# Kernel tuning notes

Measured on AMD Instinct MI355X. Metric: run time of the kernel, lower is better.

Reference implementation:

```python
import jax, jax.numpy as jnp
import numpy as np

HIDDEN = 3072
NUM_HEADS = 24
HEAD_DIM = HIDDEN // NUM_HEADS  # 128
MLP_HIDDEN = 4 * HIDDEN         # 12288
SEQ = 2048


def setup_inputs() -> dict:
    key = jax.random.key(0)
    ks = jax.random.split(key, 12)
    s = 0.02
    return {
        "x": jax.random.normal(ks[0], (1, SEQ, HIDDEN), jnp.float32),
        "vec": jax.random.normal(ks[1], (1, HIDDEN), jnp.float32),
        "pe": jax.random.normal(ks[2], (1, 1, SEQ, HEAD_DIM // 2, 2, 2), jnp.float32),
        "mod_w": jax.random.normal(ks[3], (HIDDEN, 3 * HIDDEN), jnp.float32) * s,
        "mod_b": jnp.zeros((3 * HIDDEN,), jnp.float32),
        "lin1_w": jax.random.normal(ks[4], (HIDDEN, 3 * HIDDEN + MLP_HIDDEN), jnp.float32) * s,
        "lin1_b": jnp.zeros((3 * HIDDEN + MLP_HIDDEN,), jnp.float32),
        "lin2_w": jax.random.normal(ks[5], (HIDDEN + MLP_HIDDEN, HIDDEN), jnp.float32) * s,
        "lin2_b": jnp.zeros((HIDDEN,), jnp.float32),
        "q_scale": jnp.ones((HEAD_DIM,), jnp.float32),
        "k_scale": jnp.ones((HEAD_DIM,), jnp.float32),
    }


def _forward(x, vec, pe, mod_w, mod_b, lin1_w, lin1_b, lin2_w, lin2_b, q_scale, k_scale):
    B, L, H = x.shape
    NH, HD = NUM_HEADS, HEAD_DIM

    # Modulation: lin(silu(vec)) -> shift, scale, gate  (flux Modulation, double=False)
    mod = jnp.dot(jax.nn.silu(vec), mod_w) + mod_b          # (B, 3H)
    shift, scale, gate = jnp.split(mod, 3, axis=-1)
    shift, scale, gate = shift[:, None, :], scale[:, None, :], gate[:, None, :]

    # LayerNorm (no affine, eps=1e-6) + scale/shift modulation
    mu = jnp.mean(x, axis=-1, keepdims=True)
    var = jnp.mean((x - mu) ** 2, axis=-1, keepdims=True)
    xn = (x - mu) * jax.lax.rsqrt(var + 1e-6)
    x_mod = (1.0 + scale) * xn + shift

    # Fused QKV + MLP projection
    h = jnp.dot(x_mod, lin1_w) + lin1_b                     # (B, L, 3H + MLP)
    qkv, mlp = h[..., : 3 * H], h[..., 3 * H :]
    qkv = qkv.reshape(B, L, 3, NH, HD).transpose(2, 0, 3, 1, 4)  # (3, B, NH, L, HD)
    q, k, v = qkv[0], qkv[1], qkv[2]

    # QKNorm: RMSNorm over head_dim with learned scale (eps=1e-6)
    def rms(t, s):
        return t * jax.lax.rsqrt(jnp.mean(t * t, axis=-1, keepdims=True) + 1e-6) * s

    q = rms(q, q_scale)
    k = rms(k, k_scale)

    # Rotary embedding: pe is (B, 1, L, HD/2, 2, 2) of rotation matrix rows
    def rope(t):
        tr = t.reshape(B, NH, L, HD // 2, 1, 2)
        out = pe[..., 0] * tr[..., 0] + pe[..., 1] * tr[..., 1]  # (B, NH, L, HD/2, 2)
        return out.reshape(B, NH, L, HD)

    q, k = rope(q), rope(k)

    # Scaled dot-product attention (default 1/sqrt(HD) scale)
    scores = jnp.einsum("bhqd,bhkd->bhqk", q, k) / jnp.sqrt(jnp.float32(HD))
    attn = jnp.einsum("bhqk,bhkd->bhqd", jax.nn.softmax(scores, axis=-1), v)
    attn = attn.transpose(0, 2, 1, 3).reshape(B, L, H)

    # GELU(tanh) MLP branch, concat, output projection, gated residual
    mlp_act = jax.nn.gelu(mlp, approximate=True)
    out = jnp.dot(jnp.concatenate([attn, mlp_act], axis=-1), lin2_w) + lin2_b
    return x + gate * out


def reference(x, vec, pe, mod_w, mod_b, lin1_w, lin1_b, lin2_w, lin2_b, q_scale, k_scale):
    return _forward(x, vec, pe, mod_w, mod_b, lin1_w, lin1_b, lin2_w, lin2_b, q_scale, k_scale)
```

## Files before the change

kernel.cpp:

```cpp
#include <hip/hip_runtime.h>
#include <hip/hip_bf16.h>
#include <stdint.h>

#define SEQ   2048
#define HID   3072
#define NHEADS 24
#define HDIM  128
#define MLPD  12288
#define NCOL1 21504
#define NCOL2 15360
#define MOD3  9216
#define QKVW  9216
#define KSPLIT 8

typedef __attribute__((ext_vector_type(4))) float f32x4;
typedef __attribute__((ext_vector_type(8))) short bf16x8;
typedef __attribute__((ext_vector_type(4))) unsigned short u16x4;
typedef __attribute__((ext_vector_type(2))) unsigned short u16x2;

__device__ __forceinline__ unsigned short f2bf(float f){
  unsigned u = __float_as_uint(f);
  u = (u + 0x7fffu + ((u >> 16) & 1u)) >> 16;
  return (unsigned short)u;
}
__device__ __forceinline__ float bf2f(unsigned short u){
  return __uint_as_float(((unsigned)u) << 16);
}

__device__ __forceinline__ void gload_lds16(const void* g, void* l){
  __builtin_amdgcn_global_load_lds(
      (const __attribute__((address_space(1))) unsigned int*)g,
      (__attribute__((address_space(3))) unsigned int*)l, 16, 0, 0);
}

__device__ __forceinline__ float gelu_tanh(float x){
  float u = 0.7978845608028654f * (x + 0.044715f * x * x * x);
  float t = 1.f - 2.f / (__expf(2.f * u) + 1.f);
  return 0.5f * x * (1.f + t);
}

__global__ void silu_kernel(const float* __restrict__ vec, float* __restrict__ sv){
  int i = blockIdx.x * 256 + threadIdx.x;
  if (i < HID){ float v = vec[i]; sv[i] = v / (1.f + __expf(-v)); }
}

__global__ void mod_gemv(const float* __restrict__ sv, const float* __restrict__ W,
                         const float* __restrict__ b, float* __restrict__ mod){
  int n  = blockIdx.x * 32 + (threadIdx.x & 31);
  int ks = threadIdx.x >> 5;
  float acc = 0.f;
  int k0 = ks * 384;
  #pragma unroll 4
  for (int k = k0; k < k0 + 384; ++k)
    acc += sv[k] * W[(size_t)k * MOD3 + n];
  __shared__ float red[8][32];
  red[ks][threadIdx.x & 31] = acc;
  __syncthreads();
  if (ks == 0){
    float a = 0.f;
    #pragma unroll
    for (int i = 0; i < 8; ++i) a += red[i][threadIdx.x & 31];
    mod[n] = a + b[n];
  }
}

__global__ __launch_bounds__(256)
void ln_mod_kernel(const float* __restrict__ x, const float* __restrict__ mod,
                   unsigned short* __restrict__ xmod){
  int l = blockIdx.x, t = threadIdx.x;
  const float* row = x + (size_t)l * HID;
  f32x4 v[3];
  float s = 0.f, s2 = 0.f;
  #pragma unroll
  for (int i = 0; i < 3; ++i){
    v[i] = *(const f32x4*)(row + (t + i * 256) * 4);
    #pragma unroll
    for (int j = 0; j < 4; ++j){ s += v[i][j]; s2 += v[i][j] * v[i][j]; }
  }
  #pragma unroll
  for (int m = 1; m < 64; m <<= 1){ s += __shfl_xor(s, m, 64); s2 += __shfl_xor(s2, m, 64); }
  __shared__ float red[8];
  int wv = t >> 6, ln = t & 63;
  if (ln == 0){ red[wv] = s; red[4 + wv] = s2; }
  __syncthreads();
  s  = red[0] + red[1] + red[2] + red[3];
  s2 = red[4] + red[5] + red[6] + red[7];
  float mu  = s * (1.f / HID);
  float var = s2 * (1.f / HID) - mu * mu;
  float rs  = rsqrtf(var + 1e-6f);
  #pragma unroll
  for (int i = 0; i < 3; ++i){
    int c = (t + i * 256) * 4;
    f32x4 sh = *(const f32x4*)(mod + c);
    f32x4 sc = *(const f32x4*)(mod + HID + c);
    u16x4 o;
    #pragma unroll
    for (int j = 0; j < 4; ++j){
      float xn = (v[i][j] - mu) * rs;
      o[j] = f2bf((1.f + sc[j]) * xn + sh[j]);
    }
    *(u16x4*)(xmod + (size_t)l * HID + c) = o;
  }
}

__global__ __launch_bounds__(256)
void transpose_f2b(const float* __restrict__ in, unsigned short* __restrict__ out,
                   int R, int C){
  __shared__ float tile[64][65];
  int rt = blockIdx.y * 64, ct = blockIdx.x * 64;
  int t = threadIdx.x;
  int r0 = t >> 4, c0 = (t & 15) * 4;
  #pragma unroll
  for (int ph = 0; ph < 4; ++ph){
    int r = r0 + ph * 16;
    f32x4 v = *(const f32x4*)(in + (size_t)(rt + r) * C + ct + c0);
    tile[r][c0 + 0] = v[0]; tile[r][c0 + 1] = v[1];
    tile[r][c0 + 2] = v[2]; tile[r][c0 + 3] = v[3];
  }
  __syncthreads();
  #pragma unroll
  for (int ph = 0; ph < 4; ++ph){
    int r = r0 + ph * 16;
    u16x4 o;
    #pragma unroll
    for (int i = 0; i < 4; ++i) o[i] = f2bf(tile[c0 + i][r]);
    *(u16x4*)(out + (size_t)(ct + r) * R + rt + c0) = o;
  }
}

__global__ __launch_bounds__(256)
void transpose_b2b_head(const unsigned short* __restrict__ in,
                        unsigned short* __restrict__ out, int R, int C){
  __shared__ unsigned short tile[64][68];
  int h = blockIdx.z;
  const unsigned short* inh = in + (size_t)h * R * C;
  unsigned short* outh = out + (size_t)h * R * C;
  int rt = blockIdx.y * 64, ct = blockIdx.x * 64;
  int t = threadIdx.x;
  int r0 = t >> 4, c0 = (t & 15) * 4;
  #pragma unroll
  for (int ph = 0; ph < 4; ++ph){
    int r = r0 + ph * 16;
    u16x4 v = *(const u16x4*)(inh + (size_t)(rt + r) * C + ct + c0);
    tile[r][c0 + 0] = v[0]; tile[r][c0 + 1] = v[1];
    tile[r][c0 + 2] = v[2]; tile[r][c0 + 3] = v[3];
  }
  __syncthreads();
  #pragma unroll
  for (int ph = 0; ph < 4; ++ph){
    int r = r0 + ph * 16;
    u16x4 o;
    #pragma unroll
    for (int i = 0; i < 4; ++i) o[i] = tile[c0 + i][r];
    *(u16x4*)(outh + (size_t)(ct + r) * R + rt + c0) = o;
  }
}

__global__ void qkv_prep(const unsigned short* __restrict__ hq, const float* __restrict__ pe,
                         const float* __restrict__ qscale, const float* __restrict__ kscale,
                         unsigned short* __restrict__ qb, unsigned short* __restrict__ kb,
                         unsigned short* __restrict__ vb){
  int l = blockIdx.x, hh = blockIdx.y, lane = threadIdx.x;
  const unsigned short* row = hq + (size_t)l * QKVW;
  int d = lane * 2;
  u16x2 qv = *(const u16x2*)(row + hh * HDIM + d);
  u16x2 kv = *(const u16x2*)(row + HID + hh * HDIM + d);
  u16x2 vv = *(const u16x2*)(row + 2 * HID + hh * HDIM + d);
  float qx = bf2f(qv[0]), qy = bf2f(qv[1]);
  float kx = bf2f(kv[0]), ky = bf2f(kv[1]);
  float sq = qx * qx + qy * qy;
  float sk = kx * kx + ky * ky;
  #pragma unroll
  for (int m = 1; m < 64; m <<= 1){ sq += __shfl_xor(sq, m, 64); sk += __shfl_xor(sk, m, 64); }
  float rq = rsqrtf(sq * (1.f / HDIM) + 1e-6f);
  float rk = rsqrtf(sk * (1.f / HDIM) + 1e-6f);
  float2 qs2 = *(const float2*)(qscale + d);
  float2 ks2 = *(const float2*)(kscale + d);
  float q0 = qx * rq * qs2.x, q1 = qy * rq * qs2.y;
  float k0 = kx * rk * ks2.x, k1 = ky * rk * ks2.y;
  f32x4 p4 = *(const f32x4*)(pe + (size_t)l * 256 + lane * 4);
  const float sscl = 0.08838834764831845f;
  float qo0 = (p4[0] * q0 + p4[1] * q1) * sscl;
  float qo1 = (p4[2] * q0 + p4[3] * q1) * sscl;
  float ko0 =  p4[0] * k0 + p4[1] * k1;
  float ko1 =  p4[2] * k0 + p4[3] * k1;
  size_t base = ((size_t)hh * SEQ + l) * HDIM + d;
  u16x2 o;
  o[0] = f2bf(qo0); o[1] = f2bf(qo1); *(u16x2*)(qb + base) = o;
  o[0] = f2bf(ko0); o[1] = f2bf(ko1); *(u16x2*)(kb + base) = o;
  o[0] = vv[0];     o[1] = vv[1];     *(u16x2*)(vb + base) = o;
}

template<int EPI>
__global__ __launch_bounds__(512)
void gemm256(const unsigned short* __restrict__ A, const unsigned short* __restrict__ BT,
             const float* __restrict__ bias, unsigned short* __restrict__ out0,
             unsigned short* __restrict__ out1,
             int M, int N, int ldA, int ldB, int kchunk){
  __shared__ unsigned short Ls[65536];
  int nxy = gridDim.x * gridDim.y;
  int nwg = nxy * gridDim.z;
  int fid = (blockIdx.z * gridDim.y + blockIdx.y) * gridDim.x + blockIdx.x;
  int nid = (fid & 7) * (nwg >> 3) + (fid >> 3);
  int ksz = nid / nxy, rem = nid % nxy;
  int bm  = rem % gridDim.y, bn = rem / gridDim.y;
  int k0 = ksz * kchunk;
  int nk = kchunk >> 6;
  int tid = threadIdx.x, wave = tid >> 6, lane = tid & 63, lg = lane >> 4, lr = lane & 15;
  int wr = wave >> 2, wc = wave & 3;

  int G0 = tid, G1 = tid + 512;
  int r0 = G0 >> 2, r1 = G1 >> 2;
  int c0 = ((G0 & 3) ^ ((r0 >> 1) & 3)) * 8;
  int c1 = ((G1 & 3) ^ ((r1 >> 1) & 3)) * 8;
  const unsigned short* A0 = A  + (size_t)(bm * 256 + r0) * ldA + k0 + c0;
  const unsigned short* A1 = A  + (size_t)(bm * 256 + r1) * ldA + k0 + c1;
  const unsigned short* B0 = BT + (size_t)(bn * 256 + r0) * ldB + k0 + c0;
  const unsigned short* B1 = BT + (size_t)(bn * 256 + r1) * ldB + k0 + c1;
  unsigned short* LA = Ls;
  unsigned short* LB = Ls + 32768;
  int d0 = (wave * 64) * 8, d1 = (512 + wave * 64) * 8;

  auto stageA = [&](int t, int kh){
    unsigned short* h = LA + (((t & 1) * 2 + kh) << 13);
    int kc = t * 64 + kh * 32;
    gload_lds16(A0 + kc, h + d0);
    gload_lds16(A1 + kc, h + d1);
  };
  auto stageB = [&](int t, int kh){
    unsigned short* h = LB + (((t & 1) * 2 + kh) << 13);
    int kc = t * 64 + kh * 32;
    gload_lds16(B0 + kc, h + d0);
    gload_lds16(B1 + kc, h + d1);
  };

  int offA[8], offB[4];
  #pragma unroll
  for (int m = 0; m < 8; ++m){
    int row = wr * 128 + m * 16 + lr;
    offA[m] = row * 32 + ((lg ^ ((row >> 1) & 3)) * 8);
  }
  #pragma unroll
  for (int n = 0; n < 4; ++n){
    int row = wc * 64 + n * 16 + lr;
    offB[n] = row * 32 + ((lg ^ ((row >> 1) & 3)) * 8);
  }

  const f32x4 fz = 0.0f;
  f32x4 acc[8][4];
  #pragma unroll
  for (int i = 0; i < 8; ++i)
    #pragma unroll
    for (int j = 0; j < 4; ++j) acc[i][j] = fz;

  stageA(0, 0); stageB(0, 0); stageA(0, 1); stageB(0, 1); stageA(1, 0); stageB(1, 0);
  asm volatile("s_waitcnt vmcnt(8)" ::: "memory");
  __builtin_amdgcn_s_barrier();
  __builtin_amdgcn_sched_barrier(0);

  for (int t = 0; t < nk; ++t){
    const unsigned short* Ah = LA + (((t & 1) * 2) << 13);
    const unsigned short* Bh = LB + (((t & 1) * 2) << 13);
    bf16x8 a_[4], b_[4];
    if (t + 1 < nk) stageA(t + 1, 1);
    #pragma unroll
    for (int m = 0; m < 4; ++m) a_[m] = *(const bf16x8*)&Ah[offA[m]];
    #pragma unroll
    for (int n = 0; n < 4; ++n) b_[n] = *(const bf16x8*)&Bh[offB[n]];
    __builtin_amdgcn_sched_barrier(0);
    __builtin_amdgcn_s_barrier();
    asm volatile("s_waitcnt lgkmcnt(0)" ::: "memory");
    __builtin_amdgcn_sched_barrier(0);
    __builtin_amdgcn_s_setprio(1);
    #pragma unroll
    for (int m = 0; m < 4; ++m)
      #pragma unroll
      for (int n = 0; n < 4; ++n)
        acc[m][n] = __builtin_amdgcn_mfma_f32_16x16x32_bf16(a_[m], b_[n], acc[m][n], 0, 0, 0);
    __builtin_amdgcn_s_setprio(0);
    __builtin_amdgcn_sched_barrier(0);
    __builtin_amdgcn_s_barrier();
    if (t + 1 < nk) stageB(t + 1, 1);
    #pragma unroll
    for (int m = 0; m < 4; ++m) a_[m] = *(const bf16x8*)&Ah[offA[m + 4]];
    __builtin_amdgcn_sched_barrier(0);
    if (t == nk - 1) asm volatile("s_waitcnt vmcnt(0)" ::: "memory");
    else             asm volatile("s_waitcnt vmcnt(8)" ::: "memory");
    __builtin_amdgcn_s_barrier();
    asm volatile("s_waitcnt lgkmcnt(0)" ::: "memory");
    __builtin_amdgcn_sched_barrier(0);
    __builtin_amdgcn_s_setprio(1);
    #pragma unroll
    for (int m = 0; m < 4; ++m)
      #pragma unroll
      for (int n = 0; n < 4; ++n)
        acc[m + 4][n] = __builtin_amdgcn_mfma_f32_16x16x32_bf16(a_[m], b_[n], acc[m + 4][n], 0, 0, 0);
    __builtin_amdgcn_s_setprio(0);
    __builtin_amdgcn_sched_barrier(0);
    __builtin_amdgcn_s_barrier();
    if (t + 2 < nk) stageA(t + 2, 0);
    #pragma unroll
    for (int m = 0; m < 4; ++m) a_[m] = *(const bf16x8*)&Ah[8192 + offA[m]];
    #pragma unroll
    for (int n = 0; n < 4; ++n) b_[n] = *(const bf16x8*)&Bh[8192 + offB[n]];
    __builtin_amdgcn_sched_barrier(0);
    __builtin_amdgcn_s_barrier();
    asm volatile("s_waitcnt lgkmcnt(0)" ::: "memory");
    __builtin_amdgcn_sched_barrier(0);
    __builtin_amdgcn_s_setprio(1);
    #pragma unroll
    for (int m = 0; m < 4; ++m)
      #pragma unroll
      for (int n = 0; n < 4; ++n)
        acc[m][n] = __builtin_amdgcn_mfma_f32_16x16x32_bf16(a_[m], b_[n], acc[m][n], 0, 0, 0);
    __builtin_amdgcn_s_setprio(0);
    __builtin_amdgcn_sched_barrier(0);
    __builtin_amdgcn_s_barrier();
    if (t + 2 < nk) stageB(t + 2, 0);
    #pragma unroll
    for (int m = 0; m < 4; ++m) a_[m] = *(const bf16x8*)&Ah[8192 + offA[m + 4]];
    __builtin_amdgcn_sched_barrier(0);
    if (t <= nk - 3)      asm volatile("s_waitcnt vmcnt(8)" ::: "memory");
    else if (t == nk - 2) asm volatile("s_waitcnt vmcnt(4)" ::: "memory");
    __builtin_amdgcn_s_barrier();
    asm volatile("s_waitcnt lgkmcnt(0)" ::: "memory");
    __builtin_amdgcn_sched_barrier(0);
    __builtin_amdgcn_s_setprio(1);
    #pragma unroll
    for (int m = 0; m < 4; ++m)
      #pragma unroll
      for (int n = 0; n < 4; ++n)
        acc[m + 4][n] = __builtin_amdgcn_mfma_f32_16x16x32_bf16(a_[m], b_[n], acc[m + 4][n], 0, 0, 0);
    __builtin_amdgcn_s_setprio(0);
    __builtin_amdgcn_sched_barrier(0);
    __builtin_amdgcn_s_barrier();
  }

  #pragma unroll
  for (int m = 0; m < 8; ++m)
    #pragma unroll
    for (int n = 0; n < 4; ++n){
      int col = bn * 256 + wc * 64 + n * 16 + lr;
      if constexpr (EPI == 0){
        float bv = bias[col];
        #pragma unroll
        for (int jj = 0; jj < 4; ++jj){
          int row = bm * 256 + wr * 128 + m * 16 + lg * 4 + jj;
          float r = acc[m][n][jj] + bv;
          if (col < MOD3) out0[(size_t)row * QKVW + col] = f2bf(r);
          else            out1[(size_t)row * NCOL2 + (col - 2 * HID)] = f2bf(gelu_tanh(r));
        }
      } else {
        unsigned short* P = out0 + (size_t)ksz * M * N;
        #pragma unroll
        for (int jj = 0; jj < 4; ++jj){
          int row = bm * 256 + wr * 128 + m * 16 + lg * 4 + jj;
          P[(size_t)row * N + col] = f2bf(acc[m][n][jj]);
        }
      }
    }
}

__global__ __launch_bounds__(256)
void reduce_lin2(const unsigned short* __restrict__ part, const float* __restrict__ x,
                 const float* __restrict__ gate, const float* __restrict__ bias,
                 float* __restrict__ out){
  int i4 = blockIdx.x * 256 + threadIdx.x;
  int c4 = i4 % (HID / 4);
  f32x4 s = 0.0f;
  #pragma unroll
  for (int ks = 0; ks < KSPLIT; ++ks){
    u16x4 p = *(const u16x4*)(part + (size_t)ks * SEQ * HID + (size_t)i4 * 4);
    #pragma unroll
    for (int j = 0; j < 4; ++j) s[j] += bf2f(p[j]);
  }
  f32x4 xv = *(const f32x4*)(x + (size_t)i4 * 4);
  f32x4 gv = *(const f32x4*)(gate + c4 * 4);
  f32x4 bv = *(const f32x4*)(bias + c4 * 4);
  f32x4 o;
  #pragma unroll
  for (int j = 0; j < 4; ++j) o[j] = xv[j] + gv[j] * (s[j] + bv[j]);
  *(f32x4*)(out + (size_t)i4 * 4) = o;
}

__global__ __launch_bounds__(256)
void attn_kernel(const unsigned short* __restrict__ qb, const unsigned short* __restrict__ kb,
                 const unsigned short* __restrict__ vt, unsigned short* __restrict__ a2){
  __shared__ unsigned short Ksm[64 * 128];
  __shared__ unsigned short Vsm[128 * 64];
  __shared__ unsigned short Psm[4][16 * 64];
  int fid = blockIdx.y * gridDim.x + blockIdx.x;
  int nid = (fid & 7) * 96 + (fid >> 3);
  int hh = nid / (SEQ / 64), qt = nid % (SEQ / 64);
  int tid = threadIdx.x, wave = tid >> 6, lane = tid & 63, lg = lane >> 4, lr = lane & 15;
  const unsigned short* Kh = kb + (size_t)hh * SEQ * HDIM;
  const unsigned short* Vh = vt + (size_t)hh * HDIM * SEQ;
  const unsigned short* Qh = qb + (size_t)hh * SEQ * HDIM;
  int q0 = qt * 64 + wave * 16;

  bf16x8 aq[4];
  #pragma unroll
  for (int kk = 0; kk < 4; ++kk)
    aq[kk] = *(const bf16x8*)(Qh + (size_t)(q0 + lr) * HDIM + kk * 32 + lg * 8);

  const f32x4 fzero = 0.0f;
  f32x4 acc_o[8];
  #pragma unroll
  for (int n = 0; n < 8; ++n) acc_o[n] = fzero;
  float mrun[4] = {-1e30f, -1e30f, -1e30f, -1e30f};
  float lrun[4] = {0.f, 0.f, 0.f, 0.f};

  for (int t = 0; t < SEQ / 64; ++t){
    __syncthreads();
    const unsigned short* Kt = Kh + (size_t)t * 64 * HDIM;
    const unsigned short* Vt = Vh + t * 64;
    #pragma unroll
    for (int r = 0; r < 4; ++r){
      int G  = r * 256 + tid;
      int Gs = G ^ ((G >> 4) & 7);
      gload_lds16(Kt + Gs * 8, (void*)&Ksm[(r * 256 + wave * 64) * 8]);
      int Gv = G ^ ((G >> 3) & 7);
      gload_lds16(Vt + (size_t)(Gv >> 3) * SEQ + (Gv & 7) * 8,
                  (void*)&Vsm[(r * 256 + wave * 64) * 8]);
    }
    __syncthreads();

    f32x4 sacc[4];
    #pragma unroll
    for (int j = 0; j < 4; ++j) sacc[j] = fzero;
    #pragma unroll
    for (int j = 0; j < 4; ++j){
      int kv = j * 16 + lr;
      #pragma unroll
      for (int kk = 0; kk < 4; ++kk){
        int bo = kv * 256 + (kk * 32 + lg * 8) * 2;
        bo ^= (kv & 7) << 4;
        bf16x8 bk = *(const bf16x8*)((const char*)Ksm + bo);
        sacc[j] = __builtin_amdgcn_mfma_f32_16x16x32_bf16(aq[kk], bk, sacc[j], 0, 0, 0);
      }
    }
    float scl[4], psum[4];
    #pragma unroll
    for (int jj = 0; jj < 4; ++jj){
      float m_ = fmaxf(fmaxf(sacc[0][jj], sacc[1][jj]), fmaxf(sacc[2][jj], sacc[3][jj]));
      #pragma unroll
      for (int mk = 1; mk < 16; mk <<= 1) m_ = fmaxf(m_, __shfl_xor(m_, mk, 64));
      float mn = fmaxf(mrun[jj], m_);
      scl[jj] = __expf(mrun[jj] - mn);
      mrun[jj] = mn;
      psum[jj] = 0.f;
    }
    #pragma unroll
    for (int j = 0; j < 4; ++j)
      #pragma unroll
      for (int jj = 0; jj < 4; ++jj){
        float p = __expf(sacc[j][jj] - mrun[jj]);
        sacc[j][jj] = p;
        psum[jj] += p;
      }
    #pragma unroll
    for (int jj = 0; jj < 4; ++jj){
      float ps = psum[jj];
      #pragma unroll
      for (int mk = 1; mk < 16; mk <<= 1) ps += __shfl_xor(ps, mk, 64);
      lrun[jj] = lrun[jj] * scl[jj] + ps;
    }
    #pragma unroll
    for (int n = 0; n < 8; ++n)
      #pragma unroll
      for (int jj = 0; jj < 4; ++jj) acc_o[n][jj] *= scl[jj];
    unsigned short* Pw = Psm[wave];
    #pragma unroll
    for (int j = 0; j < 4; ++j)
      #pragma unroll
      for (int jj = 0; jj < 4; ++jj){
        int prow = lg * 4 + jj, pcol = j * 16 + lr;
        int bo = prow * 128 + pcol * 2;
        bo ^= (prow & 7) << 4;
        *(unsigned short*)((char*)Pw + bo) = f2bf(sacc[j][jj]);
      }
    __syncthreads();
    #pragma unroll
    for (int k2 = 0; k2 < 2; ++k2){
      int bo = lr * 128 + (k2 * 32 + lg * 8) * 2;
      bo ^= (lr & 7) << 4;
      bf16x8 pf = *(const bf16x8*)((const char*)Pw + bo);
      #pragma unroll
      for (int n = 0; n < 8; ++n){
        int dd = n * 16 + lr;
        int vb_ = dd * 128 + (k2 * 32 + lg * 8) * 2;
        vb_ ^= (dd & 7) << 4;
        bf16x8 vf = *(const bf16x8*)((const char*)Vsm + vb_);
        acc_o[n] = __builtin_amdgcn_mfma_f32_16x16x32_bf16(pf, vf, acc_o[n], 0, 0, 0);
      }
    }
  }
  #pragma unroll
  for (int jj = 0; jj < 4; ++jj) lrun[jj] = 1.f / lrun[jj];
  #pragma unroll
  for (int n = 0; n < 8; ++n)
    #pragma unroll
    for (int jj = 0; jj < 4; ++jj){
      int row = q0 + lg * 4 + jj;
      int col = hh * HDIM + n * 16 + lr;
      a2[(size_t)row * NCOL2 + col] = f2bf(acc_o[n][jj] * lrun[jj]);
    }
}

extern "C" void kernel_launch(void* const* d_in, const int* in_sizes, int n_in,
                              void* d_out, int out_size, void* d_ws, size_t ws_size,
                              hipStream_t stream){
  const float* x       = (const float*)d_in[0];
  const float* vec     = (const float*)d_in[1];
  const float* pe      = (const float*)d_in[2];
  const float* mod_w   = (const float*)d_in[3];
  const float* mod_b   = (const float*)d_in[4];
  const float* lin1_w  = (const float*)d_in[5];
  const float* lin1_b  = (const float*)d_in[6];
  const float* lin2_w  = (const float*)d_in[7];
  const float* lin2_b  = (const float*)d_in[8];
  const float* q_scale = (const float*)d_in[9];
  const float* k_scale = (const float*)d_in[10];
  float* out = (float*)d_out;

  char* ws = (char*)d_ws;
  size_t off = 0;
  auto alloc = [&](size_t bytes){ void* p = ws + off; off += (bytes + 255) & ~(size_t)255; return p; };
  float* sv            = (float*)alloc((size_t)HID * 4);
  float* mod           = (float*)alloc((size_t)MOD3 * 4);
  unsigned short* xmod = (unsigned short*)alloc((size_t)SEQ * HID * 2);
  unsigned short* wt2  = (unsigned short*)alloc((size_t)HID * NCOL2 * 2);
  unsigned short* a2   = (unsigned short*)alloc((size_t)SEQ * NCOL2 * 2);
  unsigned short* qb   = (unsigned short*)alloc((size_t)NHEADS * SEQ * HDIM * 2);
  unsigned short* kb   = (unsigned short*)alloc((size_t)NHEADS * SEQ * HDIM * 2);
  unsigned short* vb   = (unsigned short*)alloc((size_t)NHEADS * SEQ * HDIM * 2);
  unsigned short* vt   = (unsigned short*)alloc((size_t)NHEADS * SEQ * HDIM * 2);
  unsigned short* wt1  = (unsigned short*)alloc((size_t)NCOL1 * HID * 2);
  unsigned short* hq   = (unsigned short*)alloc((size_t)SEQ * QKVW * 2);
  unsigned short* part = qb;

  silu_kernel<<<12, 256, 0, stream>>>(vec, sv);
  mod_gemv<<<MOD3 / 32, 256, 0, stream>>>(sv, mod_w, mod_b, mod);
  transpose_f2b<<<dim3(NCOL1 / 64, HID / 64), 256, 0, stream>>>(lin1_w, wt1, HID, NCOL1);
  transpose_f2b<<<dim3(HID / 64, NCOL2 / 64), 256, 0, stream>>>(lin2_w, wt2, NCOL2, HID);
  ln_mod_kernel<<<SEQ, 256, 0, stream>>>(x, mod, xmod);
  gemm256<0><<<dim3(NCOL1 / 256, SEQ / 256, 1), 512, 0, stream>>>(
      xmod, wt1, lin1_b, hq, a2, SEQ, NCOL1, HID, HID, HID);
  qkv_prep<<<dim3(SEQ, NHEADS), 64, 0, stream>>>(hq, pe, q_scale, k_scale, qb, kb, vb);
  transpose_b2b_head<<<dim3(HDIM / 64, SEQ / 64, NHEADS), 256, 0, stream>>>(vb, vt, SEQ, HDIM);
  attn_kernel<<<dim3(SEQ / 64, NHEADS), 256, 0, stream>>>(qb, kb, vt, a2);
  gemm256<2><<<dim3(HID / 256, SEQ / 256, KSPLIT), 512, 0, stream>>>(
      a2, wt2, nullptr, part, nullptr, SEQ, HID, NCOL2, NCOL2, NCOL2 / KSPLIT);
  reduce_lin2<<<SEQ * HID / 4 / 256, 256, 0, stream>>>(part, x, mod + 2 * HID, lin2_b, out);
}
```

Measured before the change: 856.4 us.

## Restructure GEMM main loop into triple-buffered 32-wide K pipeline

Replaces the double-buffered 64-wide K-step GEMM loop, which used four barriers per half-step, with a three-slot ring of 32-wide K tiles prefetched two steps ahead and a single barrier per step. LDS use drops from 128KB to 96KB. The epilogue column branch is also hoisted to the block level, since each 256-column tile is wholly QKV or wholly MLP. Risks include more loop iterations and LDS reads racing with in-flight async loads into the buffer being consumed.

```diff
diff --git a/kernel.cpp b/kernel.cpp
--- a/kernel.cpp
+++ b/kernel.cpp
@@ -17,6 +17,8 @@
 typedef __attribute__((ext_vector_type(8))) short bf16x8;
 typedef __attribute__((ext_vector_type(4))) unsigned short u16x4;
 typedef __attribute__((ext_vector_type(2))) unsigned short u16x2;
+
+#define VMC(n) asm volatile("s_waitcnt vmcnt(" #n ")" ::: "memory")
 
 __device__ __forceinline__ unsigned short f2bf(float f){
   unsigned u = __float_as_uint(f);
@@ -197,7 +199,8 @@
              const float* __restrict__ bias, unsigned short* __restrict__ out0,
              unsigned short* __restrict__ out1,
              int M, int N, int ldA, int ldB, int kchunk){
-  __shared__ unsigned short Ls[65536];
+  __shared__ unsigned short As[3 * 8192];
+  __shared__ unsigned short Bs[3 * 8192];
   int nxy = gridDim.x * gridDim.y;
   int nwg = nxy * gridDim.z;
   int fid = (blockIdx.z * gridDim.y + blockIdx.y) * gridDim.x + blockIdx.x;
@@ -205,33 +208,28 @@
   int ksz = nid / nxy, rem = nid % nxy;
   int bm  = rem % gridDim.y, bn = rem / gridDim.y;
   int k0 = ksz * kchunk;
-  int nk = kchunk >> 6;
+  int nk = kchunk >> 5;
   int tid = threadIdx.x, wave = tid >> 6, lane = tid & 63, lg = lane >> 4, lr = lane & 15;
   int wr = wave >> 2, wc = wave & 3;
 
-  int G0 = tid, G1 = tid + 512;
-  int r0 = G0 >> 2, r1 = G1 >> 2;
-  int c0 = ((G0 & 3) ^ ((r0 >> 1) & 3)) * 8;
-  int c1 = ((G1 & 3) ^ ((r1 >> 1) & 3)) * 8;
-  const unsigned short* A0 = A  + (size_t)(bm * 256 + r0) * ldA + k0 + c0;
-  const unsigned short* A1 = A  + (size_t)(bm * 256 + r1) * ldA + k0 + c1;
-  const unsigned short* B0 = BT + (size_t)(bn * 256 + r0) * ldB + k0 + c0;
-  const unsigned short* B1 = BT + (size_t)(bn * 256 + r1) * ldB + k0 + c1;
-  unsigned short* LA = Ls;
-  unsigned short* LB = Ls + 32768;
+  int rA0 = tid >> 2, rA1 = (tid + 512) >> 2;
+  int cA0 = ((tid & 3) ^ ((rA0 >> 1) & 3)) * 8;
+  int cA1 = ((tid & 3) ^ ((rA1 >> 1) & 3)) * 8;
+  const unsigned short* A0 = A  + (size_t)(bm * 256 + rA0) * ldA + k0 + cA0;
+  const unsigned short* A1 = A  + (size_t)(bm * 256 + rA1) * ldA + k0 + cA1;
+  const unsigned short* B0 = BT + (size_t)(bn * 256 + rA0) * ldB + k0 + cA0;
+  const unsigned short* B1 = BT + (size_t)(bn * 256 + rA1) * ldB + k0 + cA1;
   int d0 = (wave * 64) * 8, d1 = (512 + wave * 64) * 8;
 
-  auto stageA = [&](int t, int kh){
-    unsigned short* h = LA + (((t & 1) * 2 + kh) << 13);
-    int kc = t * 64 + kh * 32;
-    gload_lds16(A0 + kc, h + d0);
-    gload_lds16(A1 + kc, h + d1);
+  auto stageA = [&](int buf, int t){
+    unsigned short* h = As + buf * 8192;
+    gload_lds16(A0 + t * 32, h + d0);
+    gload_lds16(A1 + t * 32, h + d1);
   };
-  auto stageB = [&](int t, int kh){
-    unsigned short* h = LB + (((t & 1) * 2 + kh) << 13);
-    int kc = t * 64 + kh * 32;
-    gload_lds16(B0 + kc, h + d0);
-    gload_lds16(B1 + kc, h + d1);
+  auto stageB = [&](int buf, int t){
+    unsigned short* h = Bs + buf * 8192;
+    gload_lds16(B0 + t * 32, h + d0);
+    gload_lds16(B1 + t * 32, h + d1);
   };
 
   int offA[8], offB[4];
@@ -253,24 +251,23 @@
     #pragma unroll
     for (int j = 0; j < 4; ++j) acc[i][j] = fz;
 
-  stageA(0, 0); stageB(0, 0); stageA(0, 1); stageB(0, 1); stageA(1, 0); stageB(1, 0);
-  asm volatile("s_waitcnt vmcnt(8)" ::: "memory");
+  stageA(0, 0); stageB(0, 0); stageA(1, 1); stageB(1, 1);
+  VMC(4);
   __builtin_amdgcn_s_barrier();
   __builtin_amdgcn_sched_barrier(0);
 
+  int bc = 0;
   for (int t = 0; t < nk; ++t){
-    const unsigned short* Ah = LA + (((t & 1) * 2) << 13);
-    const unsigned short* Bh = LB + (((t & 1) * 2) << 13);
-    bf16x8 a_[4], b_[4];
-    if (t + 1 < nk) stageA(t + 1, 1);
-    #pragma unroll
-    for (int m = 0; m < 4; ++m) a_[m] = *(const bf16x8*)&Ah[offA[m]];
-    #pragma unroll
-    for (int n = 0; n < 4; ++n) b_[n] = *(const bf16x8*)&Bh[offB[n]];
+    const unsigned short* Ab = As + bc * 8192;
+    const unsigned short* Bb = Bs + bc * 8192;
+    int bs = bc + 2; if (bs >= 3) bs -= 3;
+    bf16x8 a_[4], b_[4], c_[4];
+    if (t + 2 < nk) stageA(bs, t + 2);
     __builtin_amdgcn_sched_barrier(0);
-    __builtin_amdgcn_s_barrier();
-    asm volatile("s_waitcnt lgkmcnt(0)" ::: "memory");
-    __builtin_amdgcn_sched_barrier(0);
+    #pragma unroll
+    for (int m = 0; m < 4; ++m) a_[m] = *(const bf16x8*)&Ab[offA[m]];
+    #pragma unroll
+    for (int n = 0; n < 4; ++n) b_[n] = *(const bf16x8*)&Bb[offB[n]];
     __builtin_amdgcn_s_setprio(1);
     #pragma unroll
     for (int m = 0; m < 4; ++m)
@@ -279,86 +276,66 @@
         acc[m][n] = __builtin_amdgcn_mfma_f32_16x16x32_bf16(a_[m], b_[n], acc[m][n], 0, 0, 0);
     __builtin_amdgcn_s_setprio(0);
     __builtin_amdgcn_sched_barrier(0);
-    __builtin_amdgcn_s_barrier();
-    if (t + 1 < nk) stageB(t + 1, 1);
-    #pragma unroll
-    for (int m = 0; m < 4; ++m) a_[m] = *(const bf16x8*)&Ah[offA[m + 4]];
+    if (t + 2 < nk) stageB(bs, t + 2);
     __builtin_amdgcn_sched_barrier(0);
-    if (t == nk - 1) asm volatile("s_waitcnt vmcnt(0)" ::: "memory");
-    else             asm volatile("s_waitcnt vmcnt(8)" ::: "memory");
-    __builtin_amdgcn_s_barrier();
-    asm volatile("s_waitcnt lgkmcnt(0)" ::: "memory");
-    __builtin_amdgcn_sched_barrier(0);
+    #pragma unroll
+    for (int m = 0; m < 4; ++m) c_[m] = *(const bf16x8*)&Ab[offA[m + 4]];
     __builtin_amdgcn_s_setprio(1);
     #pragma unroll
     for (int m = 0; m < 4; ++m)
       #pragma unroll
       for (int n = 0; n < 4; ++n)
-        acc[m + 4][n] = __builtin_amdgcn_mfma_f32_16x16x32_bf16(a_[m], b_[n], acc[m + 4][n], 0, 0, 0);
+        acc[m + 4][n] = __builtin_amdgcn_mfma_f32_16x16x32_bf16(c_[m], b_[n], acc[m + 4][n], 0, 0, 0);
     __builtin_amdgcn_s_setprio(0);
     __builtin_amdgcn_sched_barrier(0);
+    if (t + 2 < nk)       VMC(4);
+    else if (t + 2 == nk) VMC(0);
     __builtin_amdgcn_s_barrier();
-    if (t + 2 < nk) stageA(t + 2, 0);
-    #pragma unroll
-    for (int m = 0; m < 4; ++m) a_[m] = *(const bf16x8*)&Ah[8192 + offA[m]];
-    #pragma unroll
-    for (int n = 0; n < 4; ++n) b_[n] = *(const bf16x8*)&Bh[8192 + offB[n]];
-    __builtin_amdgcn_sched_barrier(0);
-    __builtin_amdgcn_s_barrier();
-    asm volatile("s_waitcnt lgkmcnt(0)" ::: "memory");
-    __builtin_amdgcn_sched_barrier(0);
-    __builtin_amdgcn_s_setprio(1);
-    #pragma unroll
-    for (int m = 0; m < 4; ++m)
-      #pragma unroll
-      for (int n = 0; n < 4; ++n)
-        acc[m][n] = __builtin_amdgcn_mfma_f32_16x16x32_bf16(a_[m], b_[n], acc[m][n], 0, 0, 0);
-    __builtin_amdgcn_s_setprio(0);
-    __builtin_amdgcn_sched_barrier(0);
-    __builtin_amdgcn_s_barrier();
-    if (t + 2 < nk) stageB(t + 2, 0);
-    #pragma unroll
-    for (int m = 0; m < 4; ++m) a_[m] = *(const bf16x8*)&Ah[8192 + offA[m + 4]];
-    __builtin_amdgcn_sched_barrier(0);
-    if (t <= nk - 3)      asm volatile("s_waitcnt vmcnt(8)" ::: "memory");
-    else if (t == nk - 2) asm volatile("s_waitcnt vmcnt(4)" ::: "memory");
-    __builtin_amdgcn_s_barrier();
-    asm volatile("s_waitcnt lgkmcnt(0)" ::: "memory");
-    __builtin_amdgcn_sched_barrier(0);
-    __builtin_amdgcn_s_setprio(1);
-    #pragma unroll
-    for (int m = 0; m < 4; ++m)
-      #pragma unroll
-      for (int n = 0; n < 4; ++n)
-        acc[m + 4][n] = __builtin_amdgcn_mfma_f32_16x16x32_bf16(a_[m], b_[n], acc[m + 4][n], 0, 0, 0);
-    __builtin_amdgcn_s_setprio(0);
-    __builtin_amdgcn_sched_barrier(0);
-    __builtin_amdgcn_s_barrier();
-  }
-
-  #pragma unroll
-  for (int m = 0; m < 8; ++m)
-    #pragma unroll
-    for (int n = 0; n < 4; ++n){
-      int col = bn * 256 + wc * 64 + n * 16 + lr;
-      if constexpr (EPI == 0){
-        float bv = bias[col];
+    bc = bc + 1 == 3 ? 0 : bc + 1;
+  }
+
+  if constexpr (EPI == 0){
+    if (bn < MOD3 / 256){
+      #pragma unroll
+      for (int m = 0; m < 8; ++m)
         #pragma unroll
-        for (int jj = 0; jj < 4; ++jj){
-          int row = bm * 256 + wr * 128 + m * 16 + lg * 4 + jj;
-          float r = acc[m][n][jj] + bv;
-          if (col < MOD3) out0[(size_t)row * QKVW + col] = f2bf(r);
-          else            out1[(size_t)row * NCOL2 + (col - 2 * HID)] = f2bf(gelu_tanh(r));
+        for (int n = 0; n < 4; ++n){
+          int col = bn * 256 + wc * 64 + n * 16 + lr;
+          float bv = bias[col];
+          #pragma unroll
+          for (int jj = 0; jj < 4; ++jj){
+            int row = bm * 256 + wr * 128 + m * 16 + lg * 4 + jj;
+            out0[(size_t)row * QKVW + col] = f2bf(acc[m][n][jj] + bv);
+          }
         }
-      } else {
-        unsigned short* P = out0 + (size_t)ksz * M * N;
+    } else {
+      #pragma unroll
+      for (int m = 0; m < 8; ++m)
+        #pragma unroll
+        for (int n = 0; n < 4; ++n){
+          int col = bn * 256 + wc * 64 + n * 16 + lr;
+          float bv = bias[col];
+          #pragma unroll
+          for (int jj = 0; jj < 4; ++jj){
+            int row = bm * 256 + wr * 128 + m * 16 + lg * 4 + jj;
+            out1[(size_t)row * NCOL2 + (col - 2 * HID)] = f2bf(gelu_tanh(acc[m][n][jj] + bv));
+          }
+        }
+    }
+  } else {
+    unsigned short* P = out0 + (size_t)ksz * M * N;
+    #pragma unroll
+    for (int m = 0; m < 8; ++m)
+      #pragma unroll
+      for (int n = 0; n < 4; ++n){
+        int col = bn * 256 + wc * 64 + n * 16 + lr;
         #pragma unroll
         for (int jj = 0; jj < 4; ++jj){
           int row = bm * 256 + wr * 128 + m * 16 + lg * 4 + jj;
           P[(size_t)row * N + col] = f2bf(acc[m][n][jj]);
         }
       }
-    }
+  }
 }
 
 __global__ __launch_bounds__(256)
```

Measured after the change: 957.7 us. 11.8% more time.
